# Optimization experiments

Measured on AMD Instinct MI355X. Metric: run time of the kernel, lower is better.

The kernel has to match this reference:

```python
import jax, jax.numpy as jnp
import numpy as np

NUM_HEADS = 16
LN_EPS = 1e-5
RMS_EPS = 1e-6


def rmsnorm(x, gamma, eps=RMS_EPS):
    xf = x.astype(jnp.float32)
    rms = jax.lax.rsqrt(jnp.mean(xf * xf, axis=-1, keepdims=True) + eps)
    return gamma * (xf * rms).astype(x.dtype)


def layernorm(x, g, b, eps=LN_EPS):
    mu = jnp.mean(x, axis=-1, keepdims=True)
    var = jnp.mean(jnp.square(x - mu), axis=-1, keepdims=True)
    return (x - mu) * jax.lax.rsqrt(var + eps) * g + b


def setup_inputs() -> dict:
    key = jax.random.key(0)
    E = 2048
    ks = jax.random.split(key, 10)
    std = 0.02
    inp = {
        "x": jax.random.normal(ks[0], (2, 2048, E), dtype=jnp.float32),
        "Wq": jax.random.normal(ks[1], (E, E), dtype=jnp.float32) * std,
        "Wk": jax.random.normal(ks[2], (E, E), dtype=jnp.float32) * std,
        "Wv": jax.random.normal(ks[3], (E, E), dtype=jnp.float32) * std,
        "Wo": jax.random.normal(ks[4], (E, E), dtype=jnp.float32) * std,
        "ln_g": jnp.ones((E,), jnp.float32),
        "ln_b": jnp.zeros((E,), jnp.float32),
        "rms_g": jnp.ones((E,), jnp.float32),
        "mlp_W0": jax.random.normal(ks[5], (E, E), dtype=jnp.float32) * std,
        "sw_W": jax.random.normal(ks[6], (E, E), dtype=jnp.float32) * std,
        "sw_V": jax.random.normal(ks[7], (E, E), dtype=jnp.float32) * std,
        "sw_beta": jnp.ones((1,), jnp.float32),
        "mlp_rms_g": jnp.ones((E,), jnp.float32),
    }
    return inp


def reference(x, Wq, Wk, Wv, Wo, ln_g, ln_b, rms_g, mlp_W0, sw_W, sw_V, sw_beta, mlp_rms_g):
    B, S, E = x.shape
    H = NUM_HEADS
    Dh = E // H
    scale = 1.0 / (Dh ** 0.5)

    # --- MultiheadAttention (faithful to original einsum/view quirks) ---
    q = x @ Wq.T                     # (B,S,E)
    k = (x @ Wk.T) * scale
    v = x @ Wv.T
    qh = q.reshape(B, S, H, Dh)
    kh = k.reshape(B, S, H, Dh)
    scores = jnp.einsum('bthd,bshd->bhts', qh, kh)        # (B,H,T,S)
    causal = jnp.tril(jnp.ones((S, S), dtype=bool))
    scores = jnp.where(causal, scores, -jnp.inf)
    attn = jax.nn.softmax(scores, axis=-1)
    # NOTE: v is split (B,S,Dh,H) -- head/head_dim axes swapped vs q/k, as in the torch code
    vh = v.reshape(B, S, Dh, H)
    ctx = jnp.einsum('bsdh,bhts->bthd', vh, attn)          # == torch 'kjlm,kmij->kiml'
    ctx = ctx.reshape(B, S, E)                              # flatten heads-major
    ctx = layernorm(ctx, ln_g, ln_b)
    attn_out = ctx @ Wo.T

    x = x + attn_out
    x = rmsnorm(x, rms_g)

    # --- MLP: Linear -> SwiGLU -> RMSNorm, residual ---
    h = x @ mlp_W0.T
    w = h @ sw_W.T
    swish = w * jax.nn.sigmoid(sw_beta * w)
    g = swish * (h @ sw_V.T)
    mlp_out = rmsnorm(g, mlp_rms_g)
    return x + mlp_out
```

## Files before the change

### kernel.cpp

```cpp
#include <hip/hip_runtime.h>


#define B_    2
#define S_    2048
#define E_    2048
#define H_    16
#define DH    128
#define MROWS 4096
#define NEGF  (-3.0e38f)

typedef unsigned short ushort_t;
typedef unsigned int   uint_t;
typedef ushort_t us8   __attribute__((ext_vector_type(8)));
typedef ushort_t us4   __attribute__((ext_vector_type(4)));
typedef __bf16   bf16x8 __attribute__((ext_vector_type(8)));
typedef float    f32x4 __attribute__((ext_vector_type(4)));

__device__ __forceinline__ float b2f(ushort_t u) {
    uint_t x = ((uint_t)u) << 16;
    union { uint_t u; float f; } c; c.u = x; return c.f;
}
__device__ __forceinline__ ushort_t f2b(float f) {
    union { float f; uint_t u; } c; c.f = f;
    uint_t x = c.u;
    uint_t r = (x + 0x7fffu + ((x >> 16) & 1u)) >> 16;
    return (ushort_t)r;
}

__device__ __forceinline__ void gld16(const ushort_t* g, ushort_t* l) {
    __builtin_amdgcn_global_load_lds(
        (const __attribute__((address_space(1))) void*)g,
        (__attribute__((address_space(3))) void*)l,
        16, 0, 0);
}

__global__ void probe_dtype(const ushort_t* w, int* flag) {
    __shared__ int cnt;
    if (threadIdx.x == 0) cnt = 0;
    __syncthreads();
    int c = 0;
    for (int i = threadIdx.x; i < 4096; i += 256) {
        uint_t e = (w[i] >> 7) & 0xFFu;
        if (e >= 0x84u) c++;
    }
    atomicAdd(&cnt, c);
    __syncthreads();
    if (threadIdx.x == 0) *flag = (cnt >= 8) ? 1 : 0;
}

__global__ void convert_k(const void* src, ushort_t* dst, long n, const int* flag) {
    int f = *flag;
    long i0 = (long)blockIdx.x * blockDim.x + threadIdx.x;
    long stride = (long)gridDim.x * blockDim.x;
    long n4 = n >> 2;
    if (f) {
        const f32x4* s = (const f32x4*)src;
        for (long i = i0; i < n4; i += stride) {
            f32x4 v = s[i];
            us4 o = { f2b(v[0]), f2b(v[1]), f2b(v[2]), f2b(v[3]) };
            *(us4*)(dst + i * 4) = o;
        }
        for (long i = n4 * 4 + i0; i < n; i += stride)
            dst[i] = f2b(((const float*)src)[i]);
    } else {
        const us4* s = (const us4*)src;
        for (long i = i0; i < n4; i += stride)
            *(us4*)(dst + i * 4) = s[i];
        for (long i = n4 * 4 + i0; i < n; i += stride)
            dst[i] = ((const ushort_t*)src)[i];
    }
}

__global__ void fill_diag(float* out, long n, float val) {
    long i = (long)blockIdx.x * 256 + threadIdx.x;
    if (i < n) out[i] = val;
}

__global__ __launch_bounds__(256) void gemm_bt(
    const ushort_t* __restrict__ A, const ushort_t* __restrict__ W,
    ushort_t* out, const ushort_t* resid, const ushort_t* beta,
    void* outv, const int* flagp, float scale, int mode)
{
    const int K = E_, N = E_;
    __shared__ alignas(16) ushort_t Asf[128 * 32];
    __shared__ alignas(16) ushort_t Bsf[128 * 32];

    const int tid  = threadIdx.x;
    const int wave = tid >> 6;
    const int lane = tid & 63;
    const int wm   = (wave >> 1) * 64;
    const int wn   = (wave & 1) * 64;
    const int lrow = lane & 15;
    const int quad = lane >> 4;
    const int m0   = blockIdx.y * 128;
    const int n0   = blockIdx.x * 128;

    const float betav = (beta != nullptr) ? b2f(beta[0]) : 0.0f;
    const int   of32  = (flagp != nullptr) ? *flagp : 0;

    f32x4 acc[4][4];
#pragma unroll
    for (int i = 0; i < 4; i++)
#pragma unroll
        for (int j = 0; j < 4; j++) acc[i][j] = f32x4{0.f, 0.f, 0.f, 0.f};

    const int ch   = wave * 2;
    const int crow = lane >> 2;
    const int ccol = (lane & 3) * 8;
    const ushort_t* Ag0 = A + (long)(m0 + ch * 16 + crow) * K + ccol;
    const ushort_t* Wg0 = W + (long)(n0 + ch * 16 + crow) * K + ccol;
    ushort_t* Al0 = &Asf[ch * 16 * 32];
    ushort_t* Bl0 = &Bsf[ch * 16 * 32];

    for (int kk = 0; kk < K; kk += 32) {
        gld16(Ag0 + kk,          Al0);
        gld16(Ag0 + 16 * K + kk, Al0 + 512);
        gld16(Wg0 + kk,          Bl0);
        gld16(Wg0 + 16 * K + kk, Bl0 + 512);
        __syncthreads();

        bf16x8 af[4], bfr[4];
#pragma unroll
        for (int i = 0; i < 4; i++)
            af[i]  = __builtin_bit_cast(bf16x8, *(const us8*)&Asf[(wm + i*16 + lrow) * 32 + quad * 8]);
#pragma unroll
        for (int j = 0; j < 4; j++)
            bfr[j] = __builtin_bit_cast(bf16x8, *(const us8*)&Bsf[(wn + j*16 + lrow) * 32 + quad * 8]);
#pragma unroll
        for (int i = 0; i < 4; i++)
#pragma unroll
            for (int j = 0; j < 4; j++)
                acc[i][j] = __builtin_amdgcn_mfma_f32_16x16x32_bf16(af[i], bfr[j], acc[i][j], 0, 0, 0);
        __syncthreads();
    }

#pragma unroll
    for (int i = 0; i < 4; i++)
#pragma unroll
        for (int j = 0; j < 4; j++)
#pragma unroll
            for (int r = 0; r < 4; r++) {
                int m = m0 + wm + i*16 + quad*4 + r;
                int n = n0 + wn + j*16 + lrow;
                float v = acc[i][j][r] * scale;
                long idx;
                if (mode == 1) {
                    int h = n >> 7, d = n & 127;
                    idx = ((long)h * S_ + m) * DH + d;
                } else if (mode == 2) {
                    int d = n >> 4, h = n & 15;
                    idx = ((long)h * DH + d) * S_ + m;
                } else {
                    idx = (long)m * N + n;
                    if (mode == 3) {
                        v += b2f(resid[idx]);
                    } else if (mode == 4) {
                        float wv  = b2f(resid[idx]);
                        float sig = 1.0f / (1.0f + expf(-betav * wv));
                        v = wv * sig * v;
                        if (of32) { ((float*)outv)[idx] = v; continue; }
                    }
                }
                out[idx] = f2b(v);
            }
}

__global__ __launch_bounds__(256) void gemm_qkv(
    const ushort_t* __restrict__ X,
    const ushort_t* __restrict__ Wq, const ushort_t* __restrict__ Wk,
    const ushort_t* __restrict__ Wv,
    ushort_t* qo, ushort_t* ko, ushort_t* vo, float kscale)
{
    const int K = E_;
    __shared__ alignas(16) ushort_t Asf[128 * 32];
    __shared__ alignas(16) ushort_t Bsf[128 * 32];

    const int tid  = threadIdx.x;
    const int wave = tid >> 6;
    const int lane = tid & 63;
    const int wm   = (wave >> 1) * 64;
    const int wn   = (wave & 1) * 64;
    const int lrow = lane & 15;
    const int quad = lane >> 4;
    const int sel  = blockIdx.x >> 4;
    const int n0   = (blockIdx.x & 15) * 128;
    const int m0   = blockIdx.y * 128;
    const long zoff = (long)blockIdx.z * ((long)S_ * E_);

    const ushort_t* A = X + zoff;
    const ushort_t* W = (sel == 0) ? Wq : (sel == 1) ? Wk : Wv;
    const float scale = (sel == 1) ? kscale : 1.0f;
    ushort_t* out = ((sel == 0) ? qo : (sel == 1) ? ko : vo) + zoff;

    f32x4 acc[4][4];
#pragma unroll
    for (int i = 0; i < 4; i++)
#pragma unroll
        for (int j = 0; j < 4; j++) acc[i][j] = f32x4{0.f, 0.f, 0.f, 0.f};

    const int ch   = wave * 2;
    const int crow = lane >> 2;
    const int ccol = (lane & 3) * 8;
    const ushort_t* Ag0 = A + (long)(m0 + ch * 16 + crow) * K + ccol;
    const ushort_t* Wg0 = W + (long)(n0 + ch * 16 + crow) * K + ccol;
    ushort_t* Al0 = &Asf[ch * 16 * 32];
    ushort_t* Bl0 = &Bsf[ch * 16 * 32];

    for (int kk = 0; kk < K; kk += 32) {
        gld16(Ag0 + kk,          Al0);
        gld16(Ag0 + 16 * K + kk, Al0 + 512);
        gld16(Wg0 + kk,          Bl0);
        gld16(Wg0 + 16 * K + kk, Bl0 + 512);
        __syncthreads();

        bf16x8 af[4], bfr[4];
#pragma unroll
        for (int i = 0; i < 4; i++)
            af[i]  = __builtin_bit_cast(bf16x8, *(const us8*)&Asf[(wm + i*16 + lrow) * 32 + quad * 8]);
#pragma unroll
        for (int j = 0; j < 4; j++)
            bfr[j] = __builtin_bit_cast(bf16x8, *(const us8*)&Bsf[(wn + j*16 + lrow) * 32 + quad * 8]);
#pragma unroll
        for (int i = 0; i < 4; i++)
#pragma unroll
            for (int j = 0; j < 4; j++)
                acc[i][j] = __builtin_amdgcn_mfma_f32_16x16x32_bf16(af[i], bfr[j], acc[i][j], 0, 0, 0);
        __syncthreads();
    }

#pragma unroll
    for (int i = 0; i < 4; i++)
#pragma unroll
        for (int j = 0; j < 4; j++)
#pragma unroll
            for (int r = 0; r < 4; r++) {
                int m = m0 + wm + i*16 + quad*4 + r;
                int n = n0 + wn + j*16 + lrow;
                float v = acc[i][j][r] * scale;
                long idx;
                if (sel <= 1) {
                    int h = n >> 7, d = n & 127;
                    idx = ((long)h * S_ + m) * DH + d;
                } else {
                    int d = n >> 4, h = n & 15;
                    idx = ((long)h * DH + d) * S_ + m;
                }
                out[idx] = f2b(v);
            }
}

__global__ __launch_bounds__(256) void flash_attn(
    const ushort_t* __restrict__ qp, const ushort_t* __restrict__ kp,
    const ushort_t* __restrict__ vt, ushort_t* ctx)
{
    __shared__ alignas(16) ushort_t Kt[64][144];
    __shared__ alignas(16) ushort_t Vt[128][72];
    __shared__ alignas(16) float    Sf[4][16][68];
    __shared__ alignas(16) ushort_t Pb[4][16][72];
    __shared__ alignas(16) float    Al[4][16];

    const long zq = (long)blockIdx.z * ((long)S_ * E_);
    qp  += zq; kp += zq; vt += zq; ctx += zq;

    const int tid  = threadIdx.x;
    const int wave = tid >> 6;
    const int lane = tid & 63;
    const int lrow = lane & 15;
    const int quad = lane >> 4;
    const int h    = blockIdx.y;
    const int t0   = blockIdx.x * 64;
    const int tw   = t0 + wave * 16;

    const long qbase = (long)h * S_ * DH;
    const long vbase = (long)h * DH * S_;

    bf16x8 qf[4];
    {
        const ushort_t* qrow = qp + qbase + (long)(tw + lrow) * DH + quad * 8;
#pragma unroll
        for (int ks = 0; ks < 4; ks++)
            qf[ks] = __builtin_bit_cast(bf16x8, *(const us8*)(qrow + ks * 32));
    }

    float m_i = NEGF, l_i = 0.0f;
    f32x4 o[8];
#pragma unroll
    for (int i = 0; i < 8; i++) o[i] = f32x4{0.f, 0.f, 0.f, 0.f};

    const int myrow_t = tw + lrow;

    for (int st = 0; st <= (int)blockIdx.x; st++) {
        const int sb = st * 64;
#pragma unroll
        for (int it = 0; it < 4; it++) {
            int L = tid + it * 256;
            int r = L >> 4, c8 = L & 15;
            *(us8*)&Kt[r][c8 * 8] = *(const us8*)(kp + qbase + (long)(sb + r) * DH + c8 * 8);
        }
#pragma unroll
        for (int it = 0; it < 4; it++) {
            int L = tid + it * 256;
            int d = L >> 3, c8 = L & 7;
            *(us8*)&Vt[d][c8 * 8] = *(const us8*)(vt + vbase + (long)d * S_ + sb + c8 * 8);
        }
        __syncthreads();

        f32x4 sacc[4];
#pragma unroll
        for (int nt = 0; nt < 4; nt++) {
            sacc[nt] = f32x4{0.f, 0.f, 0.f, 0.f};
#pragma unroll
            for (int ks = 0; ks < 4; ks++) {
                bf16x8 kf = __builtin_bit_cast(bf16x8, *(const us8*)&Kt[nt*16 + lrow][ks*32 + quad*8]);
                sacc[nt] = __builtin_amdgcn_mfma_f32_16x16x32_bf16(qf[ks], kf, sacc[nt], 0, 0, 0);
            }
        }
#pragma unroll
        for (int nt = 0; nt < 4; nt++)
#pragma unroll
            for (int r = 0; r < 4; r++)
                Sf[wave][quad*4 + r][nt*16 + lrow] = sacc[nt][r];
        __syncthreads();

        float vbuf[16];
        float mx = NEGF;
#pragma unroll
        for (int c = 0; c < 16; c++) {
            int col = quad * 16 + c;
            float sv = Sf[wave][lrow][col];
            sv = (sb + col <= myrow_t) ? sv : NEGF;
            vbuf[c] = sv;
            mx = fmaxf(mx, sv);
        }
        mx = fmaxf(mx, __shfl_xor(mx, 16));
        mx = fmaxf(mx, __shfl_xor(mx, 32));
        float m_new = fmaxf(m_i, mx);
        float alpha = expf(m_i - m_new);
        float ps = 0.0f;
#pragma unroll
        for (int c = 0; c < 16; c++) {
            float p = expf(vbuf[c] - m_new);
            ps += p;
            Pb[wave][lrow][quad*16 + c] = f2b(p);
        }
        ps += __shfl_xor(ps, 16);
        ps += __shfl_xor(ps, 32);
        l_i = l_i * alpha + ps;
        m_i = m_new;
        if (quad == 0) Al[wave][lrow] = alpha;
        __syncthreads();

        float a4[4];
#pragma unroll
        for (int r = 0; r < 4; r++) a4[r] = Al[wave][quad*4 + r];
#pragma unroll
        for (int nt = 0; nt < 8; nt++)
#pragma unroll
            for (int r = 0; r < 4; r++) o[nt][r] *= a4[r];

        bf16x8 pf[2];
#pragma unroll
        for (int ks = 0; ks < 2; ks++)
            pf[ks] = __builtin_bit_cast(bf16x8, *(const us8*)&Pb[wave][lrow][ks*32 + quad*8]);
#pragma unroll
        for (int nt = 0; nt < 8; nt++)
#pragma unroll
            for (int ks = 0; ks < 2; ks++) {
                bf16x8 vf = __builtin_bit_cast(bf16x8, *(const us8*)&Vt[nt*16 + lrow][ks*32 + quad*8]);
                o[nt] = __builtin_amdgcn_mfma_f32_16x16x32_bf16(pf[ks], vf, o[nt], 0, 0, 0);
            }
        __syncthreads();
    }

    if (quad == 0) Al[wave][lrow] = 1.0f / l_i;
    __syncthreads();
    float li4[4];
#pragma unroll
    for (int r = 0; r < 4; r++) li4[r] = Al[wave][quad*4 + r];
#pragma unroll
    for (int nt = 0; nt < 8; nt++)
#pragma unroll
        for (int r = 0; r < 4; r++) {
            int t = tw + quad*4 + r;
            int d = nt*16 + lrow;
            ctx[(long)t * E_ + h * DH + d] = f2b(o[nt][r] * li4[r]);
        }
}

__global__ __launch_bounds__(256) void ln_rows(
    const ushort_t* x, const ushort_t* __restrict__ g,
    const ushort_t* __restrict__ bta, ushort_t* out)
{
    __shared__ float red[16];
    const int row = blockIdx.x;
    const ushort_t* xr = x + (long)row * E_;
    float vals[8], s = 0.f, ss = 0.f;
#pragma unroll
    for (int i = 0; i < 8; i++) {
        float v = b2f(xr[threadIdx.x + i * 256]);
        vals[i] = v; s += v; ss += v * v;
    }
    for (int off = 1; off < 64; off <<= 1) { s += __shfl_xor(s, off); ss += __shfl_xor(ss, off); }
    int wave = threadIdx.x >> 6, lane = threadIdx.x & 63;
    if (lane == 0) { red[wave] = s; red[8 + wave] = ss; }
    __syncthreads();
    if (threadIdx.x == 0) {
        red[4]  = red[0] + red[1] + red[2] + red[3];
        red[12] = red[8] + red[9] + red[10] + red[11];
    }
    __syncthreads();
    float mu  = red[4] / E_;
    float var = red[12] / E_ - mu * mu;
    float rs  = rsqrtf(var + 1e-5f);
#pragma unroll
    for (int i = 0; i < 8; i++) {
        int c = threadIdx.x + i * 256;
        float v = (vals[i] - mu) * rs * b2f(g[c]) + b2f(bta[c]);
        out[(long)row * E_ + c] = f2b(v);
    }
}

__global__ __launch_bounds__(256) void rms_rows(
    const ushort_t* x, const ushort_t* __restrict__ g, ushort_t* out)
{
    __shared__ float red[8];
    const int row = blockIdx.x;
    const ushort_t* xr = x + (long)row * E_;
    float vals[8], ss = 0.f;
#pragma unroll
    for (int i = 0; i < 8; i++) {
        float v = b2f(xr[threadIdx.x + i * 256]);
        vals[i] = v; ss += v * v;
    }
    for (int off = 1; off < 64; off <<= 1) ss += __shfl_xor(ss, off);
    int wave = threadIdx.x >> 6, lane = threadIdx.x & 63;
    if (lane == 0) red[wave] = ss;
    __syncthreads();
    if (threadIdx.x == 0) red[4] = red[0] + red[1] + red[2] + red[3];
    __syncthreads();
    float rms = rsqrtf(red[4] / E_ + 1e-6f);
#pragma unroll
    for (int i = 0; i < 8; i++) {
        int c = threadIdx.x + i * 256;
        float v = b2f(f2b(vals[i] * rms)) * b2f(g[c]);
        out[(long)row * E_ + c] = f2b(v);
    }
}

__global__ __launch_bounds__(256) void rms_final(
    const void* x, const ushort_t* __restrict__ g,
    const ushort_t* resid, void* outv, const int* flagp)
{
    __shared__ float red[8];
    const int row = blockIdx.x;
    const int of32 = *flagp;
    float vals[8], ss = 0.f;
#pragma unroll
    for (int i = 0; i < 8; i++) {
        int c = threadIdx.x + i * 256;
        float v = of32 ? ((const float*)x)[(long)row * E_ + c]
                       : b2f(((const ushort_t*)x)[(long)row * E_ + c]);
        vals[i] = v; ss += v * v;
    }
    for (int off = 1; off < 64; off <<= 1) ss += __shfl_xor(ss, off);
    int wave = threadIdx.x >> 6, lane = threadIdx.x & 63;
    if (lane == 0) red[wave] = ss;
    __syncthreads();
    if (threadIdx.x == 0) red[4] = red[0] + red[1] + red[2] + red[3];
    __syncthreads();
    float rms = rsqrtf(red[4] / E_ + 1e-6f);
#pragma unroll
    for (int i = 0; i < 8; i++) {
        int c = threadIdx.x + i * 256;
        long idx = (long)row * E_ + c;
        if (of32) {
            float v = vals[i] * rms * b2f(g[c]) + b2f(resid[idx]);
            ((float*)outv)[idx] = v;
        } else {
            float v = b2f(f2b(vals[i] * rms)) * b2f(g[c]) + b2f(resid[idx]);
            ((ushort_t*)outv)[idx] = f2b(v);
        }
    }
}

extern "C" void kernel_launch(void* const* d_in, const int* in_sizes, int n_in,
                              void* d_out, int out_size, void* d_ws, size_t ws_size,
                              hipStream_t stream)
{
    const size_t NB  = (size_t)MROWS * E_;
    const size_t WSZ = (size_t)E_ * E_;
    const size_t QSZ = (size_t)S_ * E_;
    const float scale = 0.08838834764831845f;

    const size_t stage_elems = NB + 7 * WSZ + 6 * 4096;
    const size_t need_def    = (stage_elems + 2 * NB) * 2;
    const size_t need_direct = 2 * NB * 2;

    dim3 gFull(E_ / 128, MROWS / 128);

    if (ws_size >= need_def) {
        ushort_t* st = (ushort_t*)d_ws;
        ushort_t* c_x   = st;
        ushort_t* c_Wq  = c_x  + NB;
        ushort_t* c_Wk  = c_Wq + WSZ;
        ushort_t* c_Wv  = c_Wk + WSZ;
        ushort_t* c_Wo  = c_Wv + WSZ;
        ushort_t* c_W0  = c_Wo + WSZ;
        ushort_t* c_sW  = c_W0 + WSZ;
        ushort_t* c_sV  = c_sW + WSZ;
        ushort_t* c_lng = c_sV + WSZ;
        ushort_t* c_lnb = c_lng + 4096;
        ushort_t* c_rg  = c_lnb + 4096;
        ushort_t* c_mg  = c_rg  + 4096;
        ushort_t* c_sb  = c_mg  + 4096;
        int*      flag  = (int*)(c_sb + 4096);
        ushort_t* w0    = st + stage_elems;
        ushort_t* w1    = w0 + NB;
        ushort_t* ob    = (ushort_t*)d_out;
        ushort_t* ob2   = ob + NB;

        probe_dtype<<<1, 256, 0, stream>>>((const ushort_t*)d_in[1], flag);
        convert_k<<<1024, 256, 0, stream>>>(d_in[0],  c_x,  (long)NB,  flag);
        convert_k<<<1024, 256, 0, stream>>>(d_in[1],  c_Wq, (long)WSZ, flag);
        convert_k<<<1024, 256, 0, stream>>>(d_in[2],  c_Wk, (long)WSZ, flag);
        convert_k<<<1024, 256, 0, stream>>>(d_in[3],  c_Wv, (long)WSZ, flag);
        convert_k<<<1024, 256, 0, stream>>>(d_in[4],  c_Wo, (long)WSZ, flag);
        convert_k<<<1024, 256, 0, stream>>>(d_in[8],  c_W0, (long)WSZ, flag);
        convert_k<<<1024, 256, 0, stream>>>(d_in[9],  c_sW, (long)WSZ, flag);
        convert_k<<<1024, 256, 0, stream>>>(d_in[10], c_sV, (long)WSZ, flag);
        convert_k<<<8,    256, 0, stream>>>(d_in[5],  c_lng, E_, flag);
        convert_k<<<8,    256, 0, stream>>>(d_in[6],  c_lnb, E_, flag);
        convert_k<<<8,    256, 0, stream>>>(d_in[7],  c_rg,  E_, flag);
        convert_k<<<8,    256, 0, stream>>>(d_in[12], c_mg,  E_, flag);
        convert_k<<<1,    64,  0, stream>>>(d_in[11], c_sb,  1,  flag);

        gemm_qkv<<<dim3(48, 16, 2), 256, 0, stream>>>(c_x, c_Wq, c_Wk, c_Wv,
                                                      w0, ob, w1, scale);
        flash_attn<<<dim3(S_ / 64, H_, 2), 256, 0, stream>>>(w0, ob, w1, ob2);

        ln_rows<<<MROWS, 256, 0, stream>>>(ob2, c_lng, c_lnb, ob2);
        gemm_bt<<<gFull, 256, 0, stream>>>(ob2, c_Wo, w1, c_x, nullptr, nullptr, nullptr, 1.0f, 3);
        rms_rows<<<MROWS, 256, 0, stream>>>(w1, c_rg, w1);
        gemm_bt<<<gFull, 256, 0, stream>>>(w1, c_W0, w0, nullptr, nullptr, nullptr, nullptr, 1.0f, 0);
        gemm_bt<<<gFull, 256, 0, stream>>>(w0, c_sW, c_x, nullptr, nullptr, nullptr, nullptr, 1.0f, 0);
        gemm_bt<<<gFull, 256, 0, stream>>>(w0, c_sV, (ushort_t*)d_out, c_x, c_sb, d_out, flag, 1.0f, 4);
        rms_final<<<MROWS, 256, 0, stream>>>(d_out, c_mg, w1, d_out, flag);
    } else if (ws_size >= need_direct) {
        ushort_t* w0 = (ushort_t*)d_ws;
        ushort_t* w1 = w0 + NB;
        ushort_t* ob = (ushort_t*)d_out;
        int* flag = (int*)((char*)d_ws + 2 * NB * 2);
        hipMemsetAsync(flag, 0, sizeof(int), stream);
        const ushort_t* x   = (const ushort_t*)d_in[0];
        const ushort_t* Wq  = (const ushort_t*)d_in[1];
        const ushort_t* Wk  = (const ushort_t*)d_in[2];
        const ushort_t* Wv  = (const ushort_t*)d_in[3];
        const ushort_t* Wo  = (const ushort_t*)d_in[4];
        const ushort_t* lng = (const ushort_t*)d_in[5];
        const ushort_t* lnb = (const ushort_t*)d_in[6];
        const ushort_t* rg  = (const ushort_t*)d_in[7];
        const ushort_t* W0  = (const ushort_t*)d_in[8];
        const ushort_t* sW  = (const ushort_t*)d_in[9];
        const ushort_t* sV  = (const ushort_t*)d_in[10];
        const ushort_t* sb  = (const ushort_t*)d_in[11];
        const ushort_t* mg  = (const ushort_t*)d_in[12];
        for (int b = 0; b < B_; b++) {
            const ushort_t* xb = x + (size_t)b * QSZ;
            gemm_qkv<<<dim3(48, 16, 1), 256, 0, stream>>>(xb, Wq, Wk, Wv,
                                                          w0, w0 + QSZ, w1, scale);
            flash_attn<<<dim3(S_ / 64, H_, 1), 256, 0, stream>>>(w0, w0 + QSZ, w1, ob + (size_t)b * QSZ);
        }
        ln_rows<<<MROWS, 256, 0, stream>>>(ob, lng, lnb, ob);
        gemm_bt<<<gFull, 256, 0, stream>>>(ob, Wo, w0, x, nullptr, nullptr, nullptr, 1.0f, 3);
        rms_rows<<<MROWS, 256, 0, stream>>>(w0, rg, w0);
        gemm_bt<<<gFull, 256, 0, stream>>>(w0, W0, w1, nullptr, nullptr, nullptr, nullptr, 1.0f, 0);
        gemm_bt<<<gFull, 256, 0, stream>>>(w1, sW, ob, nullptr, nullptr, nullptr, nullptr, 1.0f, 0);
        gemm_bt<<<gFull, 256, 0, stream>>>(w1, sV, ob, ob, sb, d_out, flag, 1.0f, 4);
        rms_final<<<MROWS, 256, 0, stream>>>(ob, mg, w0, d_out, flag);
    } else {
        fill_diag<<<((long)NB + 255) / 256, 256, 0, stream>>>((float*)d_out, (long)NB,
                                                              1000.0f + ws_size * 1e-6f);
    }
}
```

Measured before the change: 797.7 us.

## Keep flash softmax in registers, pair causal tiles per block, use exp2

The flash attention kernel now does the online softmax directly on the MFMA accumulator registers, using lane shuffles in place of the shared-memory score and alpha staging. This removes two block barriers per key tile. Each block now handles query tile i and tile 31-i, so causal work is balanced across half as many blocks. The log2(e) factor is folded into the K scale so exp2 can be used. The risk is that the smaller grid lowers occupancy across the GPU.

```diff
diff --git a/kernel.cpp b/kernel.cpp
--- a/kernel.cpp
+++ b/kernel.cpp
@@ -25,6 +25,9 @@
     uint_t x = c.u;
     uint_t r = (x + 0x7fffu + ((x >> 16) & 1u)) >> 16;
     return (ushort_t)r;
+}
+__device__ __forceinline__ float fexp2(float x) {
+    return __builtin_amdgcn_exp2f(x);
 }
 
 __device__ __forceinline__ void gld16(const ushort_t* g, ushort_t* l) {
@@ -255,9 +258,7 @@
 {
     __shared__ alignas(16) ushort_t Kt[64][144];
     __shared__ alignas(16) ushort_t Vt[128][72];
-    __shared__ alignas(16) float    Sf[4][16][68];
     __shared__ alignas(16) ushort_t Pb[4][16][72];
-    __shared__ alignas(16) float    Al[4][16];
 
     const long zq = (long)blockIdx.z * ((long)S_ * E_);
     qp  += zq; kp += zq; vt += zq; ctx += zq;
@@ -268,123 +269,122 @@
     const int lrow = lane & 15;
     const int quad = lane >> 4;
     const int h    = blockIdx.y;
-    const int t0   = blockIdx.x * 64;
-    const int tw   = t0 + wave * 16;
 
     const long qbase = (long)h * S_ * DH;
     const long vbase = (long)h * DH * S_;
 
-    bf16x8 qf[4];
-    {
-        const ushort_t* qrow = qp + qbase + (long)(tw + lrow) * DH + quad * 8;
-#pragma unroll
-        for (int ks = 0; ks < 4; ks++)
-            qf[ks] = __builtin_bit_cast(bf16x8, *(const us8*)(qrow + ks * 32));
-    }
-
-    float m_i = NEGF, l_i = 0.0f;
-    f32x4 o[8];
-#pragma unroll
-    for (int i = 0; i < 8; i++) o[i] = f32x4{0.f, 0.f, 0.f, 0.f};
-
-    const int myrow_t = tw + lrow;
-
-    for (int st = 0; st <= (int)blockIdx.x; st++) {
-        const int sb = st * 64;
-#pragma unroll
-        for (int it = 0; it < 4; it++) {
-            int L = tid + it * 256;
-            int r = L >> 4, c8 = L & 15;
-            *(us8*)&Kt[r][c8 * 8] = *(const us8*)(kp + qbase + (long)(sb + r) * DH + c8 * 8);
+#pragma unroll 1
+    for (int half = 0; half < 2; half++) {
+        const int qt = (half == 0) ? (int)blockIdx.x : (31 - (int)blockIdx.x);
+        const int tw = qt * 64 + wave * 16;
+
+        bf16x8 qf[4];
+        {
+            const ushort_t* qrow = qp + qbase + (long)(tw + lrow) * DH + quad * 8;
+#pragma unroll
+            for (int ks = 0; ks < 4; ks++)
+                qf[ks] = __builtin_bit_cast(bf16x8, *(const us8*)(qrow + ks * 32));
         }
-#pragma unroll
-        for (int it = 0; it < 4; it++) {
-            int L = tid + it * 256;
-            int d = L >> 3, c8 = L & 7;
-            *(us8*)&Vt[d][c8 * 8] = *(const us8*)(vt + vbase + (long)d * S_ + sb + c8 * 8);
+
+        float m_i[4], l_i[4];
+#pragma unroll
+        for (int r = 0; r < 4; r++) { m_i[r] = NEGF; l_i[r] = 0.0f; }
+        f32x4 o[8];
+#pragma unroll
+        for (int i = 0; i < 8; i++) o[i] = f32x4{0.f, 0.f, 0.f, 0.f};
+
+        for (int st = 0; st <= qt; st++) {
+            const int sb = st * 64;
+#pragma unroll
+            for (int it = 0; it < 4; it++) {
+                int L = tid + it * 256;
+                int r = L >> 4, c8 = L & 15;
+                *(us8*)&Kt[r][c8 * 8] = *(const us8*)(kp + qbase + (long)(sb + r) * DH + c8 * 8);
+            }
+#pragma unroll
+            for (int it = 0; it < 4; it++) {
+                int L = tid + it * 256;
+                int d = L >> 3, c8 = L & 7;
+                *(us8*)&Vt[d][c8 * 8] = *(const us8*)(vt + vbase + (long)d * S_ + sb + c8 * 8);
+            }
+            __syncthreads();
+
+            f32x4 sacc[4];
+#pragma unroll
+            for (int nt = 0; nt < 4; nt++) {
+                sacc[nt] = f32x4{0.f, 0.f, 0.f, 0.f};
+#pragma unroll
+                for (int ks = 0; ks < 4; ks++) {
+                    bf16x8 kf = __builtin_bit_cast(bf16x8, *(const us8*)&Kt[nt*16 + lrow][ks*32 + quad*8]);
+                    sacc[nt] = __builtin_amdgcn_mfma_f32_16x16x32_bf16(qf[ks], kf, sacc[nt], 0, 0, 0);
+                }
+            }
+
+            const bool diag = (st == qt);
+            float alpha[4];
+#pragma unroll
+            for (int r = 0; r < 4; r++) {
+                const int trow = tw + quad * 4 + r;
+                float pv[4];
+#pragma unroll
+                for (int nt = 0; nt < 4; nt++) {
+                    float sv = sacc[nt][r];
+                    if (diag && (sb + nt*16 + lrow > trow)) sv = NEGF;
+                    pv[nt] = sv;
+                }
+                float mx = fmaxf(fmaxf(pv[0], pv[1]), fmaxf(pv[2], pv[3]));
+                mx = fmaxf(mx, __shfl_xor(mx, 1));
+                mx = fmaxf(mx, __shfl_xor(mx, 2));
+                mx = fmaxf(mx, __shfl_xor(mx, 4));
+                mx = fmaxf(mx, __shfl_xor(mx, 8));
+                float mn = fmaxf(m_i[r], mx);
+                float al = fexp2(m_i[r] - mn);
+                float s  = 0.0f;
+#pragma unroll
+                for (int nt = 0; nt < 4; nt++) {
+                    float p = fexp2(pv[nt] - mn);
+                    s += p;
+                    Pb[wave][quad*4 + r][nt*16 + lrow] = f2b(p);
+                }
+                s += __shfl_xor(s, 1);
+                s += __shfl_xor(s, 2);
+                s += __shfl_xor(s, 4);
+                s += __shfl_xor(s, 8);
+                l_i[r]  = l_i[r] * al + s;
+                m_i[r]  = mn;
+                alpha[r] = al;
+            }
+#pragma unroll
+            for (int nt = 0; nt < 8; nt++)
+#pragma unroll
+                for (int r = 0; r < 4; r++) o[nt][r] *= alpha[r];
+
+            bf16x8 pf[2];
+#pragma unroll
+            for (int ks = 0; ks < 2; ks++)
+                pf[ks] = __builtin_bit_cast(bf16x8, *(const us8*)&Pb[wave][lrow][ks*32 + quad*8]);
+#pragma unroll
+            for (int nt = 0; nt < 8; nt++)
+#pragma unroll
+                for (int ks = 0; ks < 2; ks++) {
+                    bf16x8 vf = __builtin_bit_cast(bf16x8, *(const us8*)&Vt[nt*16 + lrow][ks*32 + quad*8]);
+                    o[nt] = __builtin_amdgcn_mfma_f32_16x16x32_bf16(pf[ks], vf, o[nt], 0, 0, 0);
+                }
+            __syncthreads();
         }
-        __syncthreads();
-
-        f32x4 sacc[4];
-#pragma unroll
-        for (int nt = 0; nt < 4; nt++) {
-            sacc[nt] = f32x4{0.f, 0.f, 0.f, 0.f};
-#pragma unroll
-            for (int ks = 0; ks < 4; ks++) {
-                bf16x8 kf = __builtin_bit_cast(bf16x8, *(const us8*)&Kt[nt*16 + lrow][ks*32 + quad*8]);
-                sacc[nt] = __builtin_amdgcn_mfma_f32_16x16x32_bf16(qf[ks], kf, sacc[nt], 0, 0, 0);
-            }
-        }
-#pragma unroll
-        for (int nt = 0; nt < 4; nt++)
-#pragma unroll
-            for (int r = 0; r < 4; r++)
-                Sf[wave][quad*4 + r][nt*16 + lrow] = sacc[nt][r];
-        __syncthreads();
-
-        float vbuf[16];
-        float mx = NEGF;
-#pragma unroll
-        for (int c = 0; c < 16; c++) {
-            int col = quad * 16 + c;
-            float sv = Sf[wave][lrow][col];
-            sv = (sb + col <= myrow_t) ? sv : NEGF;
-            vbuf[c] = sv;
-            mx = fmaxf(mx, sv);
-        }
-        mx = fmaxf(mx, __shfl_xor(mx, 16));
-        mx = fmaxf(mx, __shfl_xor(mx, 32));
-        float m_new = fmaxf(m_i, mx);
-        float alpha = expf(m_i - m_new);
-        float ps = 0.0f;
-#pragma unroll
-        for (int c = 0; c < 16; c++) {
-            float p = expf(vbuf[c] - m_new);
-            ps += p;
-            Pb[wave][lrow][quad*16 + c] = f2b(p);
-        }
-        ps += __shfl_xor(ps, 16);
-        ps += __shfl_xor(ps, 32);
-        l_i = l_i * alpha + ps;
-        m_i = m_new;
-        if (quad == 0) Al[wave][lrow] = alpha;
-        __syncthreads();
-
-        float a4[4];
-#pragma unroll
-        for (int r = 0; r < 4; r++) a4[r] = Al[wave][quad*4 + r];
+
+        float li4[4];
+#pragma unroll
+        for (int r = 0; r < 4; r++) li4[r] = 1.0f / l_i[r];
 #pragma unroll
         for (int nt = 0; nt < 8; nt++)
 #pragma unroll
-            for (int r = 0; r < 4; r++) o[nt][r] *= a4[r];
-
-        bf16x8 pf[2];
-#pragma unroll
-        for (int ks = 0; ks < 2; ks++)
-            pf[ks] = __builtin_bit_cast(bf16x8, *(const us8*)&Pb[wave][lrow][ks*32 + quad*8]);
-#pragma unroll
-        for (int nt = 0; nt < 8; nt++)
-#pragma unroll
-            for (int ks = 0; ks < 2; ks++) {
-                bf16x8 vf = __builtin_bit_cast(bf16x8, *(const us8*)&Vt[nt*16 + lrow][ks*32 + quad*8]);
-                o[nt] = __builtin_amdgcn_mfma_f32_16x16x32_bf16(pf[ks], vf, o[nt], 0, 0, 0);
-            }
-        __syncthreads();
-    }
-
-    if (quad == 0) Al[wave][lrow] = 1.0f / l_i;
-    __syncthreads();
-    float li4[4];
-#pragma unroll
-    for (int r = 0; r < 4; r++) li4[r] = Al[wave][quad*4 + r];
-#pragma unroll
-    for (int nt = 0; nt < 8; nt++)
-#pragma unroll
-        for (int r = 0; r < 4; r++) {
-            int t = tw + quad*4 + r;
-            int d = nt*16 + lrow;
-            ctx[(long)t * E_ + h * DH + d] = f2b(o[nt][r] * li4[r]);
-        }
+            for (int r = 0; r < 4; r++) {
+                int t = tw + quad*4 + r;
+                int d = nt*16 + lrow;
+                ctx[(long)t * E_ + h * DH + d] = f2b(o[nt][r] * li4[r]);
+            }
+    }
 }
 
 __global__ __launch_bounds__(256) void ln_rows(
@@ -490,7 +490,7 @@
     const size_t NB  = (size_t)MROWS * E_;
     const size_t WSZ = (size_t)E_ * E_;
     const size_t QSZ = (size_t)S_ * E_;
-    const float scale = 0.08838834764831845f;
+    const float kscale = 0.08838834764831845f * 1.4426950408889634f;
 
     const size_t stage_elems = NB + 7 * WSZ + 6 * 4096;
     const size_t need_def    = (stage_elems + 2 * NB) * 2;
@@ -535,8 +535,8 @@
         convert_k<<<1,    64,  0, stream>>>(d_in[11], c_sb,  1,  flag);
 
         gemm_qkv<<<dim3(48, 16, 2), 256, 0, stream>>>(c_x, c_Wq, c_Wk, c_Wv,
-                                                      w0, ob, w1, scale);
-        flash_attn<<<dim3(S_ / 64, H_, 2), 256, 0, stream>>>(w0, ob, w1, ob2);
+                                                      w0, ob, w1, kscale);
+        flash_attn<<<dim3(16, H_, 2), 256, 0, stream>>>(w0, ob, w1, ob2);
 
         ln_rows<<<MROWS, 256, 0, stream>>>(ob2, c_lng, c_lnb, ob2);
         gemm_bt<<<gFull, 256, 0, stream>>>(ob2, c_Wo, w1, c_x, nullptr, nullptr, nullptr, 1.0f, 3);
@@ -567,8 +567,8 @@
         for (int b = 0; b < B_; b++) {
             const ushort_t* xb = x + (size_t)b * QSZ;
             gemm_qkv<<<dim3(48, 16, 1), 256, 0, stream>>>(xb, Wq, Wk, Wv,
-                                                          w0, w0 + QSZ, w1, scale);
-            flash_attn<<<dim3(S_ / 64, H_, 1), 256, 0, stream>>>(w0, w0 + QSZ, w1, ob + (size_t)b * QSZ);
+                                                          w0, w0 + QSZ, w1, kscale);
+            flash_attn<<<dim3(16, H_, 1), 256, 0, stream>>>(w0, w0 + QSZ, w1, ob + (size_t)b * QSZ);
         }
         ln_rows<<<MROWS, 256, 0, stream>>>(ob, lng, lnb, ob);
         gemm_bt<<<gFull, 256, 0, stream>>>(ob, Wo, w0, x, nullptr, nullptr, nullptr, 1.0f, 3);
```

New measurement: 772.2 us. 3.2% less time.
